# Performance work log

Hardware: AMD Instinct MI355X
Metric: run time of the kernel (lower is better)

Reference implementation:

```python
import jax, jax.numpy as jnp
import numpy as np

EPS = 1e-12  # matches torch F.normalize default eps


def _l2norm(x):
    n = jnp.linalg.norm(x, axis=-1, keepdims=True)
    return x / jnp.maximum(n, EPS)


def setup_inputs() -> dict:
    key = jax.random.key(0)
    k1, k2 = jax.random.split(key)
    B, Na, T, Nv, D = 16, 128, 10, 196, 256
    audio_feats = jax.random.normal(k1, (B, Na, D), dtype=jnp.float32)
    visual_feats = jax.random.normal(k2, (B, T, Nv, D), dtype=jnp.float32)
    temperature = jnp.asarray(2.0, dtype=jnp.float32)
    return {"audio_feats": audio_feats, "visual_feats": visual_feats,
            "temperature": temperature}


def reference(audio_feats, visual_feats, temperature):
    # audio_feats: (B, Na, D); visual_feats: (B, T, Nv, D)
    a = _l2norm(audio_feats)                         # (B, Na, D)
    v = _l2norm(visual_feats)                        # (B, T, Nv, D)
    # all-pairs token-level cosine sims: (Bx, By, Na, T, Nv)
    sims = jnp.einsum('xad,ytvd->xyatv', a, v) / temperature
    # aggregate: max over patches, mean over time, mean over audio tokens
    clip_sims = sims.max(axis=-1).mean(axis=-1).mean(axis=-1)  # (B, B)

    # InfoNCE on diagonal
    B = clip_sims.shape[0]
    diag = jnp.arange(B)
    log_p_a2v = jax.nn.log_softmax(clip_sims, axis=1)
    log_p_v2a = jax.nn.log_softmax(clip_sims.T, axis=1)
    losses = -(log_p_a2v[diag, diag] + log_p_v2a[diag, diag])
    contrastive_loss = 0.5 * losses.mean()

    # regularization: non-negativity pressure + temperature band [1, 3]
    neg = jnp.minimum(sims, 0.0)
    l_nonneg = jnp.mean(neg * neg)
    log_t = jnp.log(temperature)
    temp_low = jnp.maximum(-log_t, 0.0) ** 4
    temp_high = jnp.maximum(log_t - jnp.log(3.0), 0.0) ** 4
    reg_loss = l_nonneg + temp_low + temp_high

    total_loss = contrastive_loss + 0.3 * reg_loss
    return (total_loss, contrastive_loss, reg_loss)
```

## Files before the change

### kernel.cpp

```cpp
#include <hip/hip_runtime.h>
#include <stdint.h>


typedef float f32x16 __attribute__((ext_vector_type(16)));
typedef int   i32x8  __attribute__((ext_vector_type(8)));

#define WS_A_OFF  ((size_t)0)
#define WS_V_OFF  ((size_t)(1u<<20))
#define WS_CP_OFF (WS_V_OFF + (size_t)16*2560*256)

#define NINF (-3.4e38f)
#define SCL1 0x7F7F7F7F

__device__ __forceinline__ int fenc(float f) {
    int i = __float_as_int(f);
    return i >= 0 ? i : (i ^ 0x7fffffff);
}
__device__ __forceinline__ float fdec(int i) {
    return __int_as_float(i >= 0 ? i : (i ^ 0x7fffffff));
}
__device__ __forceinline__ void gld_lds16(const char* g, char* l) {
    __builtin_amdgcn_global_load_lds(
        (const __attribute__((address_space(1))) void*)g,
        (__attribute__((address_space(3))) void*)l, 16, 0, 0);
}

__global__ __launch_bounds__(256) void prep_kernel(const float* __restrict__ audio,
                                                   const float* __restrict__ visual,
                                                   char* __restrict__ ws)
{
    const int wave = blockIdx.x * 4 + (threadIdx.x >> 6);
    const int lane = threadIdx.x & 63;
    const int half = lane >> 5;
    const int sub  = lane & 31;
    const int row  = wave * 2 + half;

    float f[8];
    #pragma unroll
    for (int i = 0; i < 8; ++i) f[i] = 0.f;
    size_t dst;
    if (row < 2048) {
        const float* s = audio + (size_t)row * 256 + sub * 8;
        *(float4*)(f)     = *(const float4*)(s);
        *(float4*)(f + 4) = *(const float4*)(s + 4);
        dst = WS_A_OFF + (size_t)row * 256 + sub * 8;
    } else {
        const int vr  = row - 2048;
        const int y   = vr / 2560;
        const int rem = vr - y * 2560;
        const int t   = rem >> 8;
        const int vv  = rem & 255;
        if (vv < 196) {
            const float* s = visual + (size_t)((y*10 + t)*196 + vv) * 256 + sub * 8;
            *(float4*)(f)     = *(const float4*)(s);
            *(float4*)(f + 4) = *(const float4*)(s + 4);
        }
        dst = WS_V_OFF + (size_t)vr * 256 + (size_t)((sub ^ (vr & 31)) << 3);
    }

    float ss = 0.f;
    #pragma unroll
    for (int i = 0; i < 8; ++i) ss += f[i] * f[i];
    #pragma unroll
    for (int m = 1; m < 32; m <<= 1) ss += __shfl_xor(ss, m);
    const float sc = 1.0f / fmaxf(sqrtf(ss), 1e-12f);

    int w0 = __builtin_amdgcn_cvt_pk_fp8_f32(f[0]*sc, f[1]*sc, 0, false);
    w0     = __builtin_amdgcn_cvt_pk_fp8_f32(f[2]*sc, f[3]*sc, w0, true);
    int w1 = __builtin_amdgcn_cvt_pk_fp8_f32(f[4]*sc, f[5]*sc, 0, false);
    w1     = __builtin_amdgcn_cvt_pk_fp8_f32(f[6]*sc, f[7]*sc, w1, true);
    *(uint2*)(ws + dst) = make_uint2((unsigned)w0, (unsigned)w1);
}

#define STAGE(c_, buf_) do {                                          \
    const char* s_ = vbase + (size_t)(c_) * 16384 + tid * 16;         \
    char* d_ = &smem[buf_][0] + tid * 16;                             \
    gld_lds16(s_,         d_);         gld_lds16(s_ +  4096, d_ +  4096); \
    gld_lds16(s_ +  8192, d_ +  8192); gld_lds16(s_ + 12288, d_ + 12288); \
} while (0)

__global__ __launch_bounds__(256, 4) void main_kernel(char* __restrict__ ws)
{
    __shared__ __align__(16) char smem[2][16384];
    __shared__ int part[320];
    __shared__ float red[8];

    const int tid  = threadIdx.x;
    const int lane = tid & 63;
    const int wid  = tid >> 6;
    const int aw   = wid & 1;
    const int vw   = wid >> 1;
    const int l31  = lane & 31;
    const int hi   = lane >> 5;

    const int b = blockIdx.x;
    const int xcd = b & 7, s = b >> 3;
    const int y  = xcd * 2 + (s >> 6);
    const int x2 = (s & 63) >> 1;
    const int h  = s & 1;

    for (int i = tid; i < 320; i += 256) part[i] = (int)0x80000000;

    i32x8 af[4];
    {
        const char* ab = ws + WS_A_OFF + (size_t)(x2*64 + aw*32 + l31) * 256 + hi*32;
        #pragma unroll
        for (int m = 0; m < 4; ++m) {
            const uint4 p = *(const uint4*)(ab + m*64);
            const uint4 q = *(const uint4*)(ab + m*64 + 16);
            af[m][0] = (int)p.x; af[m][1] = (int)p.y; af[m][2] = (int)p.z; af[m][3] = (int)p.w;
            af[m][4] = (int)q.x; af[m][5] = (int)q.y; af[m][6] = (int)q.z; af[m][7] = (int)q.w;
        }
    }
    asm volatile("s_waitcnt vmcnt(0)" ::: "memory");
    __syncthreads();

    const char* vbase = ws + WS_V_OFF + ((size_t)y * 2560 + (size_t)h * 1280) * 256;

    float nn = 0.f, rmax = NINF;

    STAGE(0, 0);

    for (int c = 0; c < 20; ++c) {
        if (c < 19) {
            STAGE(c + 1, (c + 1) & 1);
            asm volatile("s_waitcnt vmcnt(4)" ::: "memory");
        } else {
            asm volatile("s_waitcnt vmcnt(0)" ::: "memory");
        }
        __builtin_amdgcn_s_barrier();

        const int f  = 2*c + vw;
        const int ft = f & 7;
        if (ft != 7) {
            const char* bb = &smem[c & 1][0] + (vw*32 + l31) * 256;

            f32x16 acc = {};
            #pragma unroll
            for (int m = 0; m < 4; ++m) {
                const uint2 r0 = *(const uint2*)(bb + (((m*8 + hi*4 + 0) ^ l31) << 3));
                const uint2 r1 = *(const uint2*)(bb + (((m*8 + hi*4 + 1) ^ l31) << 3));
                const uint2 r2 = *(const uint2*)(bb + (((m*8 + hi*4 + 2) ^ l31) << 3));
                const uint2 r3 = *(const uint2*)(bb + (((m*8 + hi*4 + 3) ^ l31) << 3));
                i32x8 va;
                va[0] = (int)r0.x; va[1] = (int)r0.y; va[2] = (int)r1.x; va[3] = (int)r1.y;
                va[4] = (int)r2.x; va[5] = (int)r2.y; va[6] = (int)r3.x; va[7] = (int)r3.y;
                acc = __builtin_amdgcn_mfma_scale_f32_32x32x64_f8f6f4(
                    va, af[m], acc, 0 , 0 ,
                    0, SCL1, 0, SCL1);
            }

            #pragma unroll
            for (int i = 0; i < 16; ++i) {
                const float g = fminf(acc[i], 0.f);
                nn = fmaf(g, g, nn);
            }
            float m;
            if (ft == 6) {
                m = fmaxf(fmaxf(acc[0], acc[1]), fmaxf(acc[2], acc[3]));
                if (hi) m = NINF;
            } else {
                float a0 = fmaxf(fmaxf(acc[0], acc[1]),   fmaxf(acc[2], acc[3]));
                float a1 = fmaxf(fmaxf(acc[4], acc[5]),   fmaxf(acc[6], acc[7]));
                float a2 = fmaxf(fmaxf(acc[8], acc[9]),   fmaxf(acc[10], acc[11]));
                float a3 = fmaxf(fmaxf(acc[12], acc[13]), fmaxf(acc[14], acc[15]));
                m = fmaxf(fmaxf(a0, a1), fmaxf(a2, a3));
            }
            rmax = fmaxf(rmax, m);
        }

        if ((c & 3) == 3) {
            const int tl = c >> 2;
            float v = fmaxf(rmax, __shfl_xor(rmax, 32));
            if (hi == 0)
                atomicMax(&part[(aw*32 + l31) * 5 + tl], fenc(v));
            rmax = NINF;
        }
        asm volatile("" ::: "memory");
        __builtin_amdgcn_s_barrier();
    }

    __syncthreads();

    float sum = 0.f;
    for (int i = tid; i < 320; i += 256) sum += fdec(part[i]);
    #pragma unroll
    for (int m = 1; m < 64; m <<= 1) {
        sum += __shfl_xor(sum, m);
        nn  += __shfl_xor(nn, m);
    }
    if (lane == 0) { red[wid] = sum; red[4 + wid] = nn; }
    __syncthreads();
    if (tid == 0) {
        float S = 0.f, N = 0.f;
        #pragma unroll
        for (int w = 0; w < 4; ++w) { S += red[w]; N += red[4 + w]; }
        float* cp = (float*)(ws + WS_CP_OFF);
        const int idx = (x2*16 + y)*2 + h;
        cp[idx]        = S;
        cp[1024 + idx] = N;
    }
}

__global__ void final_kernel(const char* __restrict__ ws,
                             const float* __restrict__ temp,
                             float* __restrict__ out)
{
    __shared__ float cs[16][17];
    __shared__ float nnred[256];
    __shared__ float lse_r[16], lse_c[16];
    const int tid = threadIdx.x;
    const float T = temp[0];
    const float* cp = (const float*)(ws + WS_CP_OFF);
    const int x = tid >> 4, yy = tid & 15;
    float sclip = 0.f;
    #pragma unroll
    for (int a = 0; a < 2; ++a)
        #pragma unroll
        for (int hh = 0; hh < 2; ++hh)
            sclip += cp[(((2*x + a)*16 + yy)*2) + hh];
    cs[x][yy] = sclip / (1280.0f * T);
    float n = 0.f;
    #pragma unroll
    for (int j = 0; j < 4; ++j) n += cp[1024 + tid + j*256];
    nnred[tid] = n;
    __syncthreads();
    for (int s = 128; s > 0; s >>= 1) {
        if (tid < s) nnred[tid] += nnred[tid + s];
        __syncthreads();
    }
    if (tid < 16) {
        float m = NINF;
        for (int j = 0; j < 16; ++j) m = fmaxf(m, cs[tid][j]);
        float s = 0.f;
        for (int j = 0; j < 16; ++j) s += expf(cs[tid][j] - m);
        lse_r[tid] = m + logf(s);
    } else if (tid < 32) {
        const int c = tid - 16;
        float m = NINF;
        for (int j = 0; j < 16; ++j) m = fmaxf(m, cs[j][c]);
        float s = 0.f;
        for (int j = 0; j < 16; ++j) s += expf(cs[j][c] - m);
        lse_c[c] = m + logf(s);
    }
    __syncthreads();
    if (tid == 0) {
        float acc = 0.f;
        for (int i = 0; i < 16; ++i)
            acc += (lse_r[i] - cs[i][i]) + (lse_c[i] - cs[i][i]);
        const float contrastive = 0.5f * acc * (1.0f / 16.0f);
        const float l_nonneg = nnred[0] / (64225280.0f * T * T);
        const float lt = logf(T);
        float tl = fmaxf(-lt, 0.f); tl = tl * tl; tl = tl * tl;
        float th = fmaxf(lt - 1.0986122886681098f, 0.f); th = th * th; th = th * th;
        const float reg = l_nonneg + tl + th;
        out[0] = contrastive + 0.3f * reg;
        out[1] = contrastive;
        out[2] = reg;
    }
}

extern "C" void kernel_launch(void* const* d_in, const int* in_sizes, int n_in,
                              void* d_out, int out_size, void* d_ws, size_t ws_size,
                              hipStream_t stream)
{
    const float* audio  = (const float*)d_in[0];
    const float* visual = (const float*)d_in[1];
    const float* temp   = (const float*)d_in[2];
    char* ws = (char*)d_ws;

    prep_kernel<<<5376, 256, 0, stream>>>(audio, visual, ws);
    main_kernel<<<1024, 256, 0, stream>>>(ws);
    final_kernel<<<1, 256, 0, stream>>>(ws, temp, (float*)d_out);
}
```

Measured before the change: 112.4 us.

## Triple-buffer visual staging, widen LDS swizzle reads, fuse final reduction via last-block

Moves the visual tile pipeline from double to triple buffering, prefetching two chunks ahead with one barrier per iteration instead of two. It also changes the LDS swizzle granularity to 16 bytes so each MFMA operand takes two 128-bit LDS reads instead of four 64-bit ones. The separate final kernel is folded into main_kernel using an atomic completion counter, so the last block computes the losses and one launch is saved. The costs are lower occupancy (launch bounds 3 instead of 4, more LDS per block) and reliance on correct fence and counter ordering.

Result: slower. 136.3 us (+21.3%).

```diff
diff --git a/kernel.cpp b/kernel.cpp
--- a/kernel.cpp
+++ b/kernel.cpp
@@ -8,6 +8,7 @@
 #define WS_A_OFF  ((size_t)0)
 #define WS_V_OFF  ((size_t)(1u<<20))
 #define WS_CP_OFF (WS_V_OFF + (size_t)16*2560*256)
+#define WS_CTR    (WS_CP_OFF + (size_t)8192)
 
 #define NINF (-3.4e38f)
 #define SCL1 0x7F7F7F7F
@@ -29,6 +30,8 @@
                                                    const float* __restrict__ visual,
                                                    char* __restrict__ ws)
 {
+    if (blockIdx.x == 0 && threadIdx.x == 0) *(int*)(ws + WS_CTR) = 0;
+
     const int wave = blockIdx.x * 4 + (threadIdx.x >> 6);
     const int lane = threadIdx.x & 63;
     const int half = lane >> 5;
@@ -55,7 +58,8 @@
             *(float4*)(f)     = *(const float4*)(s);
             *(float4*)(f + 4) = *(const float4*)(s + 4);
         }
-        dst = WS_V_OFF + (size_t)vr * 256 + (size_t)((sub ^ (vr & 31)) << 3);
+        dst = WS_V_OFF + (size_t)vr * 256
+            + (size_t)(((sub >> 1) ^ (vr & 15)) << 4) + (size_t)((sub & 1) << 3);
     }
 
     float ss = 0.f;
@@ -79,11 +83,14 @@
     gld_lds16(s_ +  8192, d_ +  8192); gld_lds16(s_ + 12288, d_ + 12288); \
 } while (0)
 
-__global__ __launch_bounds__(256, 4) void main_kernel(char* __restrict__ ws)
+__global__ __launch_bounds__(256, 3) void main_kernel(char* __restrict__ ws,
+                                                      const float* __restrict__ temp,
+                                                      float* __restrict__ out)
 {
-    __shared__ __align__(16) char smem[2][16384];
+    __shared__ __align__(16) char smem[3][16384];
     __shared__ int part[320];
     __shared__ float red[8];
+    __shared__ int lastflag;
 
     const int tid  = threadIdx.x;
     const int lane = tid & 63;
@@ -92,6 +99,7 @@
     const int vw   = wid >> 1;
     const int l31  = lane & 31;
     const int hi   = lane >> 5;
+    const int s16  = l31 & 15;
 
     const int b = blockIdx.x;
     const int xcd = b & 7, s = b >> 3;
@@ -112,42 +120,32 @@
             af[m][4] = (int)q.x; af[m][5] = (int)q.y; af[m][6] = (int)q.z; af[m][7] = (int)q.w;
         }
     }
-    asm volatile("s_waitcnt vmcnt(0)" ::: "memory");
-    __syncthreads();
 
     const char* vbase = ws + WS_V_OFF + ((size_t)y * 2560 + (size_t)h * 1280) * 256;
 
+    STAGE(0, 0);
+    STAGE(1, 1);
+    __syncthreads();
+
     float nn = 0.f, rmax = NINF;
 
-    STAGE(0, 0);
-
+    int bc = 0;
     for (int c = 0; c < 20; ++c) {
-        if (c < 19) {
-            STAGE(c + 1, (c + 1) & 1);
-            asm volatile("s_waitcnt vmcnt(4)" ::: "memory");
-        } else {
-            asm volatile("s_waitcnt vmcnt(0)" ::: "memory");
-        }
-        __builtin_amdgcn_s_barrier();
-
         const int f  = 2*c + vw;
         const int ft = f & 7;
         if (ft != 7) {
-            const char* bb = &smem[c & 1][0] + (vw*32 + l31) * 256;
+            const char* bb = &smem[bc][0] + (vw*32 + l31) * 256;
 
             f32x16 acc = {};
             #pragma unroll
             for (int m = 0; m < 4; ++m) {
-                const uint2 r0 = *(const uint2*)(bb + (((m*8 + hi*4 + 0) ^ l31) << 3));
-                const uint2 r1 = *(const uint2*)(bb + (((m*8 + hi*4 + 1) ^ l31) << 3));
-                const uint2 r2 = *(const uint2*)(bb + (((m*8 + hi*4 + 2) ^ l31) << 3));
-                const uint2 r3 = *(const uint2*)(bb + (((m*8 + hi*4 + 3) ^ l31) << 3));
+                const uint4 q0 = *(const uint4*)(bb + (((m*4 + hi*2    ) ^ s16) << 4));
+                const uint4 q1 = *(const uint4*)(bb + (((m*4 + hi*2 + 1) ^ s16) << 4));
                 i32x8 va;
-                va[0] = (int)r0.x; va[1] = (int)r0.y; va[2] = (int)r1.x; va[3] = (int)r1.y;
-                va[4] = (int)r2.x; va[5] = (int)r2.y; va[6] = (int)r3.x; va[7] = (int)r3.y;
+                va[0] = (int)q0.x; va[1] = (int)q0.y; va[2] = (int)q0.z; va[3] = (int)q0.w;
+                va[4] = (int)q1.x; va[5] = (int)q1.y; va[6] = (int)q1.z; va[7] = (int)q1.w;
                 acc = __builtin_amdgcn_mfma_scale_f32_32x32x64_f8f6f4(
-                    va, af[m], acc, 0 , 0 ,
-                    0, SCL1, 0, SCL1);
+                    va, af[m], acc, 0 , 0 , 0, SCL1, 0, SCL1);
             }
 
             #pragma unroll
@@ -168,7 +166,6 @@
             }
             rmax = fmaxf(rmax, m);
         }
-
         if ((c & 3) == 3) {
             const int tl = c >> 2;
             float v = fmaxf(rmax, __shfl_xor(rmax, 32));
@@ -176,8 +173,17 @@
                 atomicMax(&part[(aw*32 + l31) * 5 + tl], fenc(v));
             rmax = NINF;
         }
-        asm volatile("" ::: "memory");
-        __builtin_amdgcn_s_barrier();
+
+        if (c + 2 < 20) {
+            const int bs = (bc + 2 >= 3) ? bc - 1 : bc + 2;
+            STAGE(c + 2, bs);
+        }
+        if (c < 19) {
+            if (c == 18) asm volatile("s_waitcnt vmcnt(0)" ::: "memory");
+            else         asm volatile("s_waitcnt vmcnt(4)" ::: "memory");
+            __builtin_amdgcn_s_barrier();
+        }
+        bc = (bc + 1 == 3) ? 0 : bc + 1;
     }
 
     __syncthreads();
@@ -191,63 +197,64 @@
     }
     if (lane == 0) { red[wid] = sum; red[4 + wid] = nn; }
     __syncthreads();
+    float* cp = (float*)(ws + WS_CP_OFF);
     if (tid == 0) {
         float S = 0.f, N = 0.f;
         #pragma unroll
         for (int w = 0; w < 4; ++w) { S += red[w]; N += red[4 + w]; }
-        float* cp = (float*)(ws + WS_CP_OFF);
         const int idx = (x2*16 + y)*2 + h;
         cp[idx]        = S;
         cp[1024 + idx] = N;
-    }
-}
-
-__global__ void final_kernel(const char* __restrict__ ws,
-                             const float* __restrict__ temp,
-                             float* __restrict__ out)
-{
-    __shared__ float cs[16][17];
-    __shared__ float nnred[256];
-    __shared__ float lse_r[16], lse_c[16];
-    const int tid = threadIdx.x;
+        __threadfence();
+        const int old = atomicAdd((int*)(ws + WS_CTR), 1);
+        lastflag = (old == 1023) ? 1 : 0;
+    }
+    __syncthreads();
+    if (lastflag == 0) return;
+
+    __threadfence();
+    float* fs     = (float*)&smem[0][0];
+    float* cs     = fs;
+    float* nnred  = fs + 272;
+    float* lse_r  = fs + 528;
+    float* lse_c  = fs + 544;
     const float T = temp[0];
-    const float* cp = (const float*)(ws + WS_CP_OFF);
-    const int x = tid >> 4, yy = tid & 15;
+    const int xr = tid >> 4, yy = tid & 15;
     float sclip = 0.f;
     #pragma unroll
     for (int a = 0; a < 2; ++a)
         #pragma unroll
         for (int hh = 0; hh < 2; ++hh)
-            sclip += cp[(((2*x + a)*16 + yy)*2) + hh];
-    cs[x][yy] = sclip / (1280.0f * T);
+            sclip += cp[(((2*xr + a)*16 + yy)*2) + hh];
+    cs[xr*17 + yy] = sclip / (1280.0f * T);
     float n = 0.f;
     #pragma unroll
     for (int j = 0; j < 4; ++j) n += cp[1024 + tid + j*256];
     nnred[tid] = n;
     __syncthreads();
-    for (int s = 128; s > 0; s >>= 1) {
-        if (tid < s) nnred[tid] += nnred[tid + s];
+    for (int sr = 128; sr > 0; sr >>= 1) {
+        if (tid < sr) nnred[tid] += nnred[tid + sr];
         __syncthreads();
     }
     if (tid < 16) {
         float m = NINF;
-        for (int j = 0; j < 16; ++j) m = fmaxf(m, cs[tid][j]);
-        float s = 0.f;
-        for (int j = 0; j < 16; ++j) s += expf(cs[tid][j] - m);
-        lse_r[tid] = m + logf(s);
+        for (int j = 0; j < 16; ++j) m = fmaxf(m, cs[tid*17 + j]);
+        float sv = 0.f;
+        for (int j = 0; j < 16; ++j) sv += expf(cs[tid*17 + j] - m);
+        lse_r[tid] = m + logf(sv);
     } else if (tid < 32) {
-        const int c = tid - 16;
+        const int cc = tid - 16;
         float m = NINF;
-        for (int j = 0; j < 16; ++j) m = fmaxf(m, cs[j][c]);
-        float s = 0.f;
-        for (int j = 0; j < 16; ++j) s += expf(cs[j][c] - m);
-        lse_c[c] = m + logf(s);
+        for (int j = 0; j < 16; ++j) m = fmaxf(m, cs[j*17 + cc]);
+        float sv = 0.f;
+        for (int j = 0; j < 16; ++j) sv += expf(cs[j*17 + cc] - m);
+        lse_c[cc] = m + logf(sv);
     }
     __syncthreads();
     if (tid == 0) {
         float acc = 0.f;
         for (int i = 0; i < 16; ++i)
-            acc += (lse_r[i] - cs[i][i]) + (lse_c[i] - cs[i][i]);
+            acc += (lse_r[i] - cs[i*17 + i]) + (lse_c[i] - cs[i*17 + i]);
         const float contrastive = 0.5f * acc * (1.0f / 16.0f);
         const float l_nonneg = nnred[0] / (64225280.0f * T * T);
         const float lt = logf(T);
@@ -270,6 +277,5 @@
     char* ws = (char*)d_ws;
 
     prep_kernel<<<5376, 256, 0, stream>>>(audio, visual, ws);
-    main_kernel<<<1024, 256, 0, stream>>>(ws);
-    final_kernel<<<1, 256, 0, stream>>>(ws, temp, (float*)d_out);
-}
+    main_kernel<<<1024, 256, 0, stream>>>(ws, temp, (float*)d_out);
+}
```
